# Performance work log

Measured on AMD Instinct MI355X. Metric: run time of the kernel, lower is better.

Reference implementation:

```python
import jax, jax.numpy as jnp
import numpy as np
from jax import lax

MEL = 80
HID = 512
NCLS = 64
B = 16
T = 1000


def setup_inputs() -> dict:
    key = jax.random.key(0)
    ks = jax.random.split(key, 16)
    s_in = 1.0 / np.sqrt(MEL)
    s_h = 1.0 / np.sqrt(HID)
    return {
        'feats': jax.random.normal(ks[0], (B, T, MEL), jnp.float32),
        'C0': jax.random.normal(ks[1], (MEL, HID), jnp.float32) * s_h,
        'B0': jax.random.normal(ks[2], (HID, MEL), jnp.float32) * s_in,
        'W0': jax.random.normal(ks[3], (HID, MEL), jnp.float32) * s_in,
        'a0': jax.random.normal(ks[4], (HID,), jnp.float32) * 0.1,
        'tau00': jnp.array([0.5], jnp.float32),
        'gamma0': jnp.array([0.25], jnp.float32),
        'C1': jax.random.normal(ks[5], (HID, HID), jnp.float32) * s_h,
        'B1': jax.random.normal(ks[6], (HID, HID), jnp.float32) * s_h,
        'W1': jax.random.normal(ks[7], (HID, HID), jnp.float32) * s_h,
        'a1': jax.random.normal(ks[8], (HID,), jnp.float32) * 0.1,
        'tau01': jnp.array([0.5], jnp.float32),
        'gamma1': jnp.array([0.25], jnp.float32),
        'head_w': jax.random.normal(ks[9], (NCLS, 2 * HID), jnp.float32) * (1.0 / np.sqrt(2 * HID)),
        'head_b': jnp.zeros((NCLS,), jnp.float32),
    }


def _cell_step(h, x_t, C, Bm, Wm, a, tau0, gamma):
    # x_t: (B, in_dim), h: (B, HID)
    x_scale = jnp.maximum(jnp.linalg.norm(x_t, axis=-1, keepdims=True), 1e-6)  # (B,1)
    x_norm = jnp.clip(x_t / x_scale, -1.0, 1.0)
    hd = lax.stop_gradient(h)
    error = x_t - jnp.tanh(hd @ C.T) * x_scale                                 # (B, in_dim)
    rel_err = jnp.minimum(jnp.linalg.norm(error, axis=-1) / lax.stop_gradient(x_scale[:, 0]), 4.0)
    surprise = jax.nn.sigmoid((rel_err - tau0[0]) / gamma[0])                   # (B,)
    base_eff = x_norm @ Bm.T                                                    # (B, HID)
    err_eff = error @ Wm.T                                                      # (B, HID)
    input_h = hd * 0.2 + base_eff * 0.6 + err_eff * surprise[:, None] * 0.2
    # liquid-time-constant update: surprise-gated leaky integration toward tanh(input_h)
    g = surprise[:, None] * jax.nn.sigmoid(a)[None, :]                          # (B, HID) in (0,1)
    h_new = h * (1.0 - g) + jnp.tanh(input_h) * g
    return h_new, base_eff


def reference(feats, C0, B0, W0, a0, tau00, gamma0, C1, B1, W1, a1, tau01, gamma1, head_w, head_b):
    Bsz = feats.shape[0]
    feats_t = jnp.swapaxes(feats, 0, 1)  # (T, B, MEL)
    h0_init = jnp.zeros((Bsz, HID), feats.dtype)
    h1_init = jnp.zeros((Bsz, HID), feats.dtype)

    def scan_fn(carry, x_t):
        h0, h1 = carry
        h0n, be0 = _cell_step(h0, x_t, C0, B0, W0, a0, tau00, gamma0)
        h1n, be1 = _cell_step(h1, be0, C1, B1, W1, a1, tau01, gamma1)
        return (h0n, h1n), jnp.concatenate([h1n, be1], axis=-1)

    _, ys = lax.scan(scan_fn, (h0_init, h1_init), feats_t)  # (T, B, 2*HID)
    stacked = jnp.swapaxes(ys, 0, 1)                        # (B, T, 2*HID)
    return stacked @ head_w.T + head_b                      # (B, T, NCLS)
```

## Files before the change

kernel.cpp:

```cpp
#include <hip/hip_runtime.h>
#include <math.h>

#define T_LEN 1000
#define BATCH 16
#define MEL   80
#define HID   512
#define NCLS  64
#define SL    8

__device__ __forceinline__ float fast_tanh(float x) {
    float e = __expf(2.0f * x);
    return 1.0f - 2.0f / (e + 1.0f);
}
__device__ __forceinline__ float fast_sigmoid(float x) {
    return 1.0f / (1.0f + __expf(-x));
}

__device__ __forceinline__ unsigned long long pack_pair(float v, unsigned e) {
    return ((unsigned long long)e << 32) | (unsigned long long)__float_as_uint(v);
}
__device__ __forceinline__ float pair_val(unsigned long long p) {
    return __uint_as_float((unsigned)(p & 0xffffffffull));
}
__device__ __forceinline__ unsigned pair_epoch(unsigned long long p) {
    return (unsigned)(p >> 32);
}

__device__ __forceinline__ void llc_load16c(const float* base, float4 (&r)[16]) {
    asm volatile(
        "global_load_dwordx4 %0, %16, off sc0 sc1\n\t"
        "global_load_dwordx4 %1, %16, off offset:16 sc0 sc1\n\t"
        "global_load_dwordx4 %2, %16, off offset:32 sc0 sc1\n\t"
        "global_load_dwordx4 %3, %16, off offset:48 sc0 sc1\n\t"
        "global_load_dwordx4 %4, %16, off offset:64 sc0 sc1\n\t"
        "global_load_dwordx4 %5, %16, off offset:80 sc0 sc1\n\t"
        "global_load_dwordx4 %6, %16, off offset:96 sc0 sc1\n\t"
        "global_load_dwordx4 %7, %16, off offset:112 sc0 sc1\n\t"
        "global_load_dwordx4 %8, %16, off offset:128 sc0 sc1\n\t"
        "global_load_dwordx4 %9, %16, off offset:144 sc0 sc1\n\t"
        "global_load_dwordx4 %10, %16, off offset:160 sc0 sc1\n\t"
        "global_load_dwordx4 %11, %16, off offset:176 sc0 sc1\n\t"
        "global_load_dwordx4 %12, %16, off offset:192 sc0 sc1\n\t"
        "global_load_dwordx4 %13, %16, off offset:208 sc0 sc1\n\t"
        "global_load_dwordx4 %14, %16, off offset:224 sc0 sc1\n\t"
        "global_load_dwordx4 %15, %16, off offset:240 sc0 sc1\n\t"
        "s_waitcnt vmcnt(0)"
        : "=&v"(r[0]), "=&v"(r[1]), "=&v"(r[2]), "=&v"(r[3]),
          "=&v"(r[4]), "=&v"(r[5]), "=&v"(r[6]), "=&v"(r[7]),
          "=&v"(r[8]), "=&v"(r[9]), "=&v"(r[10]), "=&v"(r[11]),
          "=&v"(r[12]), "=&v"(r[13]), "=&v"(r[14]), "=&v"(r[15])
        : "v"(base)
        : "memory");
}

#define PART_WORDS (BATCH * 2 * SL * HID)
__global__ void k0_init(unsigned long long* part) {
    int i = blockIdx.x * 256 + threadIdx.x;
    if (i < PART_WORDS) part[i] = 0ull;
}

__global__ __launch_bounds__(256) void k1_be0(const float* __restrict__ feats,
                                              const float* __restrict__ B0,
                                              float* __restrict__ be0) {
    const int t = blockIdx.x;
    const int tid = threadIdx.x;
    __shared__ float xf[BATCH][MEL];
    __shared__ float sc[BATCH];
    for (int idx = tid; idx < BATCH * MEL; idx += 256) {
        int b = idx / MEL, m = idx % MEL;
        xf[b][m] = feats[b * (T_LEN * MEL) + t * MEL + m];
    }
    __syncthreads();
    if (tid < BATCH) {
        float ss = 0.f;
        for (int m = 0; m < MEL; ++m) { float v = xf[tid][m]; ss += v * v; }
        sc[tid] = fmaxf(sqrtf(ss), 1e-6f);
    }
    __syncthreads();
    for (int idx = tid; idx < BATCH * MEL; idx += 256) {
        int b = idx / MEL, m = idx % MEL;
        float v = xf[b][m] / sc[b];
        xf[b][m] = fminf(fmaxf(v, -1.f), 1.f);
    }
    __syncthreads();
    for (int j = tid; j < HID; j += 256) {
        float acc[BATCH];
        #pragma unroll
        for (int b = 0; b < BATCH; ++b) acc[b] = 0.f;
        const float* brow = B0 + j * MEL;
        for (int k = 0; k < MEL; k += 4) {
            float4 w = *(const float4*)(brow + k);
            #pragma unroll
            for (int b = 0; b < BATCH; ++b) {
                float4 xv = *(const float4*)(&xf[b][k]);
                acc[b] += w.x * xv.x + w.y * xv.y + w.z * xv.z + w.w * xv.w;
            }
        }
        #pragma unroll
        for (int b = 0; b < BATCH; ++b)
            be0[(t * BATCH + b) * HID + j] = acc[b];
    }
}

__global__ __launch_bounds__(512, 1) void k3_fused(
    const float* __restrict__ be0g,
    const float* __restrict__ C1, const float* __restrict__ W1,
    const float* __restrict__ B1,
    const float* __restrict__ a1, const float* __restrict__ tau,
    const float* __restrict__ gam,
    float* __restrict__ be1g, float* __restrict__ h1s,
    unsigned long long* part)
{
    const int chain = blockIdx.x & 15;
    const int slice = blockIdx.x >> 4;
    const int tid = threadIdx.x;
    const int w = tid >> 6;
    const int lane = tid & 63;
    const int jq = tid >> 3;
    const int kc = tid & 7;
    const int j2 = slice * 64 + jq;
    const bool lead = (kc == 0);

    float4 wC[16], wW[16], wB[16];
    llc_load16c(C1 + (size_t)tid * HID + slice * 64, wC);
    llc_load16c(W1 + (size_t)j2 * HID + kc * 64, wW);
    llc_load16c(B1 + (size_t)j2 * HID + kc * 64, wB);

    const float tauv = tau[0], gamv = gam[0];
    const float siga = fast_sigmoid(a1[j2]);

    unsigned long long* pc = part + (size_t)chain * (2 * SL * HID);

    __shared__ float h_s[64];
    __shared__ __align__(16) float e_s[HID + 32];
    __shared__ __align__(16) float x_s[HID + 32];
    __shared__ float sq_s[8];
    __shared__ float xsq_s[8];

    float hj = 0.f;
    if (tid < 64) h_s[tid] = 0.f;

    float cur_be0 = be0g[(size_t)chain * HID + tid];
    float cur_xs, cur_be1 = 0.f;
    {
        float sq = cur_be0 * cur_be0;
        #pragma unroll
        for (int off = 32; off > 0; off >>= 1) sq += __shfl_down(sq, off, 64);
        if (lane == 0) xsq_s[w] = sq;
        __syncthreads();
        float ssX = ((xsq_s[0] + xsq_s[1]) + (xsq_s[2] + xsq_s[3]))
                  + ((xsq_s[4] + xsq_s[5]) + (xsq_s[6] + xsq_s[7]));
        cur_xs = fmaxf(sqrtf(ssX), 1e-6f);
        float xn = cur_be0 / cur_xs;
        x_s[tid + (tid >> 6) * 4] = fminf(fmaxf(xn, -1.f), 1.f);
        __syncthreads();
        const float* xb = x_s + kc * 68;
        float q0 = 0.f, q1 = 0.f, q2 = 0.f, q3 = 0.f;
        #pragma unroll
        for (int i = 0; i < 16; ++i) {
            float4 v4 = *(const float4*)(xb + 4 * i);
            q0 += wB[i].x * v4.x; q1 += wB[i].y * v4.y;
            q2 += wB[i].z * v4.z; q3 += wB[i].w * v4.w;
        }
        float bq = (q0 + q1) + (q2 + q3);
        bq += __shfl_down(bq, 4, 8);
        bq += __shfl_down(bq, 2, 8);
        bq += __shfl_down(bq, 1, 8);
        if (lead) {
            cur_be1 = bq;
            __builtin_nontemporal_store(bq, &be1g[(size_t)chain * HID + j2]);
        }
        __syncthreads();
    }

    for (int t = 0; t < T_LEN; ++t) {
        float nxt_be0 = 0.f;
        if (t + 1 < T_LEN)
            nxt_be0 = be0g[(size_t)((t + 1) * BATCH + chain) * HID + tid];
        const unsigned tag = (unsigned)(t + 1);
        unsigned long long* ps = pc + (size_t)(t & 1) * (SL * HID);

        {
            float p0 = 0.f, p1 = 0.f, p2 = 0.f, p3 = 0.f;
            #pragma unroll
            for (int i = 0; i < 16; ++i) {
                float4 hv = *(const float4*)(h_s + 4 * i);
                p0 += wC[i].x * hv.x; p1 += wC[i].y * hv.y;
                p2 += wC[i].z * hv.z; p3 += wC[i].w * hv.w;
            }
            float pp = (p0 + p1) + (p2 + p3);
            __hip_atomic_store(&ps[slice * HID + tid], pack_pair(pp, tag),
                               __ATOMIC_RELAXED, __HIP_MEMORY_SCOPE_AGENT);
        }

        float nxt_xs = 0.f, nxt_be1 = 0.f;
        if (t + 1 < T_LEN) {
            float sq = nxt_be0 * nxt_be0;
            #pragma unroll
            for (int off = 32; off > 0; off >>= 1) sq += __shfl_down(sq, off, 64);
            if (lane == 0) xsq_s[w] = sq;
            __syncthreads();
            float ssX = ((xsq_s[0] + xsq_s[1]) + (xsq_s[2] + xsq_s[3]))
                      + ((xsq_s[4] + xsq_s[5]) + (xsq_s[6] + xsq_s[7]));
            nxt_xs = fmaxf(sqrtf(ssX), 1e-6f);
            float xn = nxt_be0 / nxt_xs;
            x_s[tid + (tid >> 6) * 4] = fminf(fmaxf(xn, -1.f), 1.f);
            __syncthreads();
            const float* xb = x_s + kc * 68;
            float q0 = 0.f, q1 = 0.f, q2 = 0.f, q3 = 0.f;
            #pragma unroll
            for (int i = 0; i < 16; ++i) {
                float4 v4 = *(const float4*)(xb + 4 * i);
                q0 += wB[i].x * v4.x; q1 += wB[i].y * v4.y;
                q2 += wB[i].z * v4.z; q3 += wB[i].w * v4.w;
            }
            float bq = (q0 + q1) + (q2 + q3);
            bq += __shfl_down(bq, 4, 8);
            bq += __shfl_down(bq, 2, 8);
            bq += __shfl_down(bq, 1, 8);
            if (lead) {
                nxt_be1 = bq;
                __builtin_nontemporal_store(bq,
                    &be1g[(size_t)((t + 1) * BATCH + chain) * HID + j2]);
            }
        }

        float dp;
        {
            const unsigned long long* a0 = ps + 0 * HID + tid;
            const unsigned long long* a1p = ps + 1 * HID + tid;
            const unsigned long long* a2 = ps + 2 * HID + tid;
            const unsigned long long* a3 = ps + 3 * HID + tid;
            const unsigned long long* a4 = ps + 4 * HID + tid;
            const unsigned long long* a5 = ps + 5 * HID + tid;
            const unsigned long long* a6 = ps + 6 * HID + tid;
            const unsigned long long* a7 = ps + 7 * HID + tid;
            unsigned long long q0, q1, q2, q3, q4, q5, q6, q7;
            int rounds = 0;
            for (;;) {
                asm volatile(
                    "global_load_dwordx2 %0, %8, off sc0 sc1\n\t"
                    "global_load_dwordx2 %1, %9, off sc0 sc1\n\t"
                    "global_load_dwordx2 %2, %10, off sc0 sc1\n\t"
                    "global_load_dwordx2 %3, %11, off sc0 sc1\n\t"
                    "global_load_dwordx2 %4, %12, off sc0 sc1\n\t"
                    "global_load_dwordx2 %5, %13, off sc0 sc1\n\t"
                    "global_load_dwordx2 %6, %14, off sc0 sc1\n\t"
                    "global_load_dwordx2 %7, %15, off sc0 sc1\n\t"
                    "s_waitcnt vmcnt(0)"
                    : "=&v"(q0), "=&v"(q1), "=&v"(q2), "=&v"(q3),
                      "=&v"(q4), "=&v"(q5), "=&v"(q6), "=&v"(q7)
                    : "v"(a0), "v"(a1p), "v"(a2), "v"(a3),
                      "v"(a4), "v"(a5), "v"(a6), "v"(a7)
                    : "memory");
                bool ok = (pair_epoch(q0) == tag) & (pair_epoch(q1) == tag)
                        & (pair_epoch(q2) == tag) & (pair_epoch(q3) == tag)
                        & (pair_epoch(q4) == tag) & (pair_epoch(q5) == tag)
                        & (pair_epoch(q6) == tag) & (pair_epoch(q7) == tag);
                if (__all(ok)) break;
                if (++rounds > 200000) {
                    q0 = __hip_atomic_load(a0, __ATOMIC_RELAXED, __HIP_MEMORY_SCOPE_AGENT);
                    q1 = __hip_atomic_load(a1p, __ATOMIC_RELAXED, __HIP_MEMORY_SCOPE_AGENT);
                    q2 = __hip_atomic_load(a2, __ATOMIC_RELAXED, __HIP_MEMORY_SCOPE_AGENT);
                    q3 = __hip_atomic_load(a3, __ATOMIC_RELAXED, __HIP_MEMORY_SCOPE_AGENT);
                    q4 = __hip_atomic_load(a4, __ATOMIC_RELAXED, __HIP_MEMORY_SCOPE_AGENT);
                    q5 = __hip_atomic_load(a5, __ATOMIC_RELAXED, __HIP_MEMORY_SCOPE_AGENT);
                    q6 = __hip_atomic_load(a6, __ATOMIC_RELAXED, __HIP_MEMORY_SCOPE_AGENT);
                    q7 = __hip_atomic_load(a7, __ATOMIC_RELAXED, __HIP_MEMORY_SCOPE_AGENT);
                    bool ok2 = (pair_epoch(q0) == tag) & (pair_epoch(q1) == tag)
                             & (pair_epoch(q2) == tag) & (pair_epoch(q3) == tag)
                             & (pair_epoch(q4) == tag) & (pair_epoch(q5) == tag)
                             & (pair_epoch(q6) == tag) & (pair_epoch(q7) == tag);
                    if (__all(ok2)) break;
                    rounds = 0;
                }
                __builtin_amdgcn_s_sleep(1);
            }
            dp = ((pair_val(q0) + pair_val(q1)) + (pair_val(q2) + pair_val(q3)))
               + ((pair_val(q4) + pair_val(q5)) + (pair_val(q6) + pair_val(q7)));
        }

        {
            float err = cur_be0 - fast_tanh(dp) * cur_xs;
            e_s[tid + (tid >> 6) * 4] = err;
            float sq = err * err;
            #pragma unroll
            for (int off = 32; off > 0; off >>= 1) sq += __shfl_down(sq, off, 64);
            if (lane == 0) sq_s[w] = sq;
        }
        __syncthreads();

        {
            float ssT = ((sq_s[0] + sq_s[1]) + (sq_s[2] + sq_s[3]))
                      + ((sq_s[4] + sq_s[5]) + (sq_s[6] + sq_s[7]));
            const float* esb = e_s + kc * 68;
            float q0 = 0.f, q1 = 0.f, q2 = 0.f, q3 = 0.f;
            #pragma unroll
            for (int i = 0; i < 16; ++i) {
                float4 ev = *(const float4*)(esb + 4 * i);
                q0 += wW[i].x * ev.x; q1 += wW[i].y * ev.y;
                q2 += wW[i].z * ev.z; q3 += wW[i].w * ev.w;
            }
            float ee = (q0 + q1) + (q2 + q3);
            ee += __shfl_down(ee, 4, 8);
            ee += __shfl_down(ee, 2, 8);
            ee += __shfl_down(ee, 1, 8);
            if (lead) {
                float rel = fminf(sqrtf(ssT) / cur_xs, 4.0f);
                float s = fast_sigmoid((rel - tauv) / gamv);
                float input_h = hj * 0.2f + cur_be1 * 0.6f + ee * s * 0.2f;
                float g = s * siga;
                hj = hj * (1.f - g) + fast_tanh(input_h) * g;
                h_s[jq] = hj;
                __builtin_nontemporal_store(hj,
                    &h1s[(size_t)(t * BATCH + chain) * HID + j2]);
            }
        }
        __syncthreads();

        cur_be0 = nxt_be0; cur_be1 = nxt_be1; cur_xs = nxt_xs;
    }
}

__global__ __launch_bounds__(512) void k4_head(const float* __restrict__ h1s,
                                               const float* __restrict__ be1,
                                               const float* __restrict__ head_w,
                                               const float* __restrict__ head_b,
                                               float* __restrict__ out) {
    const int t = blockIdx.x;
    const int tid = threadIdx.x;
    const int c = tid >> 3;
    const int kc = tid & 7;

    float4 wA[16], wB4[16];
    llc_load16c(head_w + (size_t)c * (2 * HID) + kc * 128, wA);
    llc_load16c(head_w + (size_t)c * (2 * HID) + kc * 128 + 64, wB4);
    const float hb = head_b[c];

    __shared__ __align__(16) float xs[BATCH * 1056];

    const float* src1 = h1s + (size_t)t * BATCH * HID;
    const float* src2 = be1 + (size_t)t * BATCH * HID;
    #pragma unroll
    for (int j = 0; j < 8; ++j) {
        int fidx = tid + j * 512;
        int b = fidx >> 8;
        int r = fidx & 255;
        int k0 = r * 4;
        float4 v = (k0 < HID)
                 ? *(const float4*)(src1 + (size_t)b * HID + k0)
                 : *(const float4*)(src2 + (size_t)b * HID + (k0 - HID));
        *(float4*)(&xs[b * 1056 + k0 + (k0 >> 7) * 4]) = v;
    }
    __syncthreads();

    #pragma unroll
    for (int b = 0; b < BATCH; ++b) {
        const float* xb = xs + b * 1056 + kc * 132;
        float q0 = 0.f, q1 = 0.f, q2 = 0.f, q3 = 0.f;
        #pragma unroll
        for (int i = 0; i < 16; ++i) {
            float4 v4 = *(const float4*)(xb + 4 * i);
            q0 += wA[i].x * v4.x; q1 += wA[i].y * v4.y;
            q2 += wA[i].z * v4.z; q3 += wA[i].w * v4.w;
        }
        #pragma unroll
        for (int i = 0; i < 16; ++i) {
            float4 v4 = *(const float4*)(xb + 64 + 4 * i);
            q0 += wB4[i].x * v4.x; q1 += wB4[i].y * v4.y;
            q2 += wB4[i].z * v4.z; q3 += wB4[i].w * v4.w;
        }
        float p = (q0 + q1) + (q2 + q3);
        p += __shfl_down(p, 4, 8);
        p += __shfl_down(p, 2, 8);
        p += __shfl_down(p, 1, 8);
        if (kc == 0)
            out[b * (T_LEN * NCLS) + t * NCLS + c] = p + hb;
    }
}

extern "C" void kernel_launch(void* const* d_in, const int* in_sizes, int n_in,
                              void* d_out, int out_size, void* d_ws, size_t ws_size,
                              hipStream_t stream) {
    const float* feats  = (const float*)d_in[0];
    const float* B0     = (const float*)d_in[2];
    const float* C1     = (const float*)d_in[7];
    const float* B1     = (const float*)d_in[8];
    const float* W1     = (const float*)d_in[9];
    const float* a1     = (const float*)d_in[10];
    const float* tau1   = (const float*)d_in[11];
    const float* gam1   = (const float*)d_in[12];
    const float* head_w = (const float*)d_in[13];
    const float* head_b = (const float*)d_in[14];
    float* out = (float*)d_out;

    float* be0 = (float*)d_ws;
    float* be1 = be0 + (size_t)T_LEN * BATCH * HID;
    float* h1s = be1 + (size_t)T_LEN * BATCH * HID;
    unsigned long long* part =
        (unsigned long long*)(h1s + (size_t)T_LEN * BATCH * HID);

    hipLaunchKernelGGL(k0_init, dim3(512), dim3(256), 0, stream, part);
    hipLaunchKernelGGL(k1_be0, dim3(T_LEN), dim3(256), 0, stream, feats, B0, be0);
    hipLaunchKernelGGL(k3_fused, dim3(BATCH * SL), dim3(512), 0, stream,
                       be0, C1, W1, B1, a1, tau1, gam1, be1, h1s, part);
    hipLaunchKernelGGL(k4_head, dim3(T_LEN), dim3(512), 0, stream,
                       h1s, be1, head_w, head_b, out);
}
```

Measured before the change: 3.487 ms.

## Fuse layer-0 input projection into the recurrent kernel and drop k1_be0

Removes the separate k1_be0 kernel and the be0 workspace buffer. Each recurrent block now loads its row of B0 into registers and computes be0 for the next timestep directly from feats. This avoids a kernel launch and the write and re-read of a 32 MB intermediate. In exchange, every step inside the serial time loop gains two extra __syncthreads and an 80-wide dot product, and register pressure rises by about 80 floats per thread.

```diff
diff --git a/kernel.cpp b/kernel.cpp
--- a/kernel.cpp
+++ b/kernel.cpp
@@ -53,59 +53,28 @@
         : "memory");
 }
 
+__device__ __forceinline__ void llc_load4c(const float* base, float4 (&r)[4]) {
+    asm volatile(
+        "global_load_dwordx4 %0, %4, off sc0 sc1\n\t"
+        "global_load_dwordx4 %1, %4, off offset:16 sc0 sc1\n\t"
+        "global_load_dwordx4 %2, %4, off offset:32 sc0 sc1\n\t"
+        "global_load_dwordx4 %3, %4, off offset:48 sc0 sc1\n\t"
+        "s_waitcnt vmcnt(0)"
+        : "=&v"(r[0]), "=&v"(r[1]), "=&v"(r[2]), "=&v"(r[3])
+        : "v"(base)
+        : "memory");
+}
+
 #define PART_WORDS (BATCH * 2 * SL * HID)
 __global__ void k0_init(unsigned long long* part) {
     int i = blockIdx.x * 256 + threadIdx.x;
     if (i < PART_WORDS) part[i] = 0ull;
 }
 
-__global__ __launch_bounds__(256) void k1_be0(const float* __restrict__ feats,
-                                              const float* __restrict__ B0,
-                                              float* __restrict__ be0) {
-    const int t = blockIdx.x;
-    const int tid = threadIdx.x;
-    __shared__ float xf[BATCH][MEL];
-    __shared__ float sc[BATCH];
-    for (int idx = tid; idx < BATCH * MEL; idx += 256) {
-        int b = idx / MEL, m = idx % MEL;
-        xf[b][m] = feats[b * (T_LEN * MEL) + t * MEL + m];
-    }
-    __syncthreads();
-    if (tid < BATCH) {
-        float ss = 0.f;
-        for (int m = 0; m < MEL; ++m) { float v = xf[tid][m]; ss += v * v; }
-        sc[tid] = fmaxf(sqrtf(ss), 1e-6f);
-    }
-    __syncthreads();
-    for (int idx = tid; idx < BATCH * MEL; idx += 256) {
-        int b = idx / MEL, m = idx % MEL;
-        float v = xf[b][m] / sc[b];
-        xf[b][m] = fminf(fmaxf(v, -1.f), 1.f);
-    }
-    __syncthreads();
-    for (int j = tid; j < HID; j += 256) {
-        float acc[BATCH];
-        #pragma unroll
-        for (int b = 0; b < BATCH; ++b) acc[b] = 0.f;
-        const float* brow = B0 + j * MEL;
-        for (int k = 0; k < MEL; k += 4) {
-            float4 w = *(const float4*)(brow + k);
-            #pragma unroll
-            for (int b = 0; b < BATCH; ++b) {
-                float4 xv = *(const float4*)(&xf[b][k]);
-                acc[b] += w.x * xv.x + w.y * xv.y + w.z * xv.z + w.w * xv.w;
-            }
-        }
-        #pragma unroll
-        for (int b = 0; b < BATCH; ++b)
-            be0[(t * BATCH + b) * HID + j] = acc[b];
-    }
-}
-
 __global__ __launch_bounds__(512, 1) void k3_fused(
-    const float* __restrict__ be0g,
+    const float* __restrict__ feats,
     const float* __restrict__ C1, const float* __restrict__ W1,
-    const float* __restrict__ B1,
+    const float* __restrict__ B1, const float* __restrict__ B0,
     const float* __restrict__ a1, const float* __restrict__ tau,
     const float* __restrict__ gam,
     float* __restrict__ be1g, float* __restrict__ h1s,
@@ -121,28 +90,67 @@
     const int j2 = slice * 64 + jq;
     const bool lead = (kc == 0);
 
-    float4 wC[16], wW[16], wB[16];
+    float4 wC[16], wW[16], wB[16], wB0a[16], wB0b[4];
     llc_load16c(C1 + (size_t)tid * HID + slice * 64, wC);
     llc_load16c(W1 + (size_t)j2 * HID + kc * 64, wW);
     llc_load16c(B1 + (size_t)j2 * HID + kc * 64, wB);
+    llc_load16c(B0 + (size_t)tid * MEL, wB0a);
+    llc_load4c(B0 + (size_t)tid * MEL + 64, wB0b);
 
     const float tauv = tau[0], gamv = gam[0];
     const float siga = fast_sigmoid(a1[j2]);
 
     unsigned long long* pc = part + (size_t)chain * (2 * SL * HID);
+    const float* frow = feats + (size_t)chain * T_LEN * MEL;
 
     __shared__ float h_s[64];
     __shared__ __align__(16) float e_s[HID + 32];
     __shared__ __align__(16) float x_s[HID + 32];
+    __shared__ __align__(16) float4 xf4_s[20];
+    __shared__ float fsq_s[20];
+    __shared__ __align__(16) float xn0_s[80];
     __shared__ float sq_s[8];
     __shared__ float xsq_s[8];
 
     float hj = 0.f;
     if (tid < 64) h_s[tid] = 0.f;
 
-    float cur_be0 = be0g[(size_t)chain * HID + tid];
-    float cur_xs, cur_be1 = 0.f;
+    float cur_be0, cur_xs, cur_be1 = 0.f;
     {
+        if (tid < 20) {
+            float4 fv = *(const float4*)(frow + tid * 4);
+            xf4_s[tid] = fv;
+            fsq_s[tid] = fv.x*fv.x + fv.y*fv.y + fv.z*fv.z + fv.w*fv.w;
+        }
+        __syncthreads();
+        if (tid < 20) {
+            float ss = 0.f;
+            #pragma unroll
+            for (int i = 0; i < 20; ++i) ss += fsq_s[i];
+            float inv = 1.f / fmaxf(sqrtf(ss), 1e-6f);
+            float4 v = xf4_s[tid];
+            v.x = fminf(fmaxf(v.x * inv, -1.f), 1.f);
+            v.y = fminf(fmaxf(v.y * inv, -1.f), 1.f);
+            v.z = fminf(fmaxf(v.z * inv, -1.f), 1.f);
+            v.w = fminf(fmaxf(v.w * inv, -1.f), 1.f);
+            *(float4*)(&xn0_s[tid * 4]) = v;
+        }
+        __syncthreads();
+        float acc = 0.f;
+        #pragma unroll
+        for (int i = 0; i < 16; ++i) {
+            float4 xv = *(const float4*)(&xn0_s[4 * i]);
+            acc += wB0a[i].x * xv.x + wB0a[i].y * xv.y
+                 + wB0a[i].z * xv.z + wB0a[i].w * xv.w;
+        }
+        #pragma unroll
+        for (int i = 0; i < 4; ++i) {
+            float4 xv = *(const float4*)(&xn0_s[64 + 4 * i]);
+            acc += wB0b[i].x * xv.x + wB0b[i].y * xv.y
+                 + wB0b[i].z * xv.z + wB0b[i].w * xv.w;
+        }
+        cur_be0 = acc;
+
         float sq = cur_be0 * cur_be0;
         #pragma unroll
         for (int off = 32; off > 0; off >>= 1) sq += __shfl_down(sq, off, 64);
@@ -174,9 +182,9 @@
     }
 
     for (int t = 0; t < T_LEN; ++t) {
-        float nxt_be0 = 0.f;
-        if (t + 1 < T_LEN)
-            nxt_be0 = be0g[(size_t)((t + 1) * BATCH + chain) * HID + tid];
+        float4 fv = make_float4(0.f, 0.f, 0.f, 0.f);
+        if (t + 1 < T_LEN && tid < 20)
+            fv = *(const float4*)(frow + (size_t)(t + 1) * MEL + tid * 4);
         const unsigned tag = (unsigned)(t + 1);
         unsigned long long* ps = pc + (size_t)(t & 1) * (SL * HID);
 
@@ -193,8 +201,42 @@
                                __ATOMIC_RELAXED, __HIP_MEMORY_SCOPE_AGENT);
         }
 
-        float nxt_xs = 0.f, nxt_be1 = 0.f;
+        float nxt_be0 = 0.f, nxt_xs = 0.f, nxt_be1 = 0.f;
         if (t + 1 < T_LEN) {
+            if (tid < 20) {
+                xf4_s[tid] = fv;
+                fsq_s[tid] = fv.x*fv.x + fv.y*fv.y + fv.z*fv.z + fv.w*fv.w;
+            }
+            __syncthreads();
+            if (tid < 20) {
+                float ss = 0.f;
+                #pragma unroll
+                for (int i = 0; i < 20; ++i) ss += fsq_s[i];
+                float inv = 1.f / fmaxf(sqrtf(ss), 1e-6f);
+                float4 v = xf4_s[tid];
+                v.x = fminf(fmaxf(v.x * inv, -1.f), 1.f);
+                v.y = fminf(fmaxf(v.y * inv, -1.f), 1.f);
+                v.z = fminf(fmaxf(v.z * inv, -1.f), 1.f);
+                v.w = fminf(fmaxf(v.w * inv, -1.f), 1.f);
+                *(float4*)(&xn0_s[tid * 4]) = v;
+            }
+            __syncthreads();
+            {
+                float acc = 0.f;
+                #pragma unroll
+                for (int i = 0; i < 16; ++i) {
+                    float4 xv = *(const float4*)(&xn0_s[4 * i]);
+                    acc += wB0a[i].x * xv.x + wB0a[i].y * xv.y
+                         + wB0a[i].z * xv.z + wB0a[i].w * xv.w;
+                }
+                #pragma unroll
+                for (int i = 0; i < 4; ++i) {
+                    float4 xv = *(const float4*)(&xn0_s[64 + 4 * i]);
+                    acc += wB0b[i].x * xv.x + wB0b[i].y * xv.y
+                         + wB0b[i].z * xv.z + wB0b[i].w * xv.w;
+                }
+                nxt_be0 = acc;
+            }
             float sq = nxt_be0 * nxt_be0;
             #pragma unroll
             for (int off = 32; off > 0; off >>= 1) sq += __shfl_down(sq, off, 64);
@@ -394,16 +436,14 @@
     const float* head_b = (const float*)d_in[14];
     float* out = (float*)d_out;
 
-    float* be0 = (float*)d_ws;
-    float* be1 = be0 + (size_t)T_LEN * BATCH * HID;
+    float* be1 = (float*)d_ws;
     float* h1s = be1 + (size_t)T_LEN * BATCH * HID;
     unsigned long long* part =
         (unsigned long long*)(h1s + (size_t)T_LEN * BATCH * HID);
 
     hipLaunchKernelGGL(k0_init, dim3(512), dim3(256), 0, stream, part);
-    hipLaunchKernelGGL(k1_be0, dim3(T_LEN), dim3(256), 0, stream, feats, B0, be0);
     hipLaunchKernelGGL(k3_fused, dim3(BATCH * SL), dim3(512), 0, stream,
-                       be0, C1, W1, B1, a1, tau1, gam1, be1, h1s, part);
+                       feats, C1, W1, B1, B0, a1, tau1, gam1, be1, h1s, part);
     hipLaunchKernelGGL(k4_head, dim3(T_LEN), dim3(512), 0, stream,
                        h1s, be1, head_w, head_b, out);
 }
```

Measured after the change: 9.161 ms. +162.7%, slower.
